# Performance work log

Measured on AMD Instinct MI355X. Metric: run time of the kernel, lower is better.

Reference implementation:

```python
import jax, jax.numpy as jnp
import numpy as np
from jax import lax

E = 64        # SUB_NETWORK_DIM
M = 512       # memory_size
H = 8         # num_heads
DH = E // H
B = 32768     # batch of x
EPS = 1e-5


def setup_inputs() -> dict:
    key = jax.random.key(0)
    ks = jax.random.split(key, 12)
    inp = {
        "x": jax.random.normal(ks[0], (B, E), jnp.float32),
        # MemoryModule params (torch.randn init)
        "mem_w": jax.random.normal(ks[1], (M, E, E), jnp.float32),
        "ln_g": jnp.ones((M, E), jnp.float32),
        "ln_b": jnp.zeros((M, E), jnp.float32),
        # pre-attention projections
        "Wq": jax.random.normal(ks[2], (E, E), jnp.float32) * 0.05,
        "bq": jnp.zeros((E,), jnp.float32),
        "Wk": jax.random.normal(ks[3], (E, E), jnp.float32) * 0.05,
        "bk": jnp.zeros((E,), jnp.float32),
        "Wv": jax.random.normal(ks[4], (E, E), jnp.float32) * 0.05,
        "bv": jnp.zeros((E,), jnp.float32),
        # nn.MultiheadAttention internal projections
        "in_proj_w": jax.random.normal(ks[5], (3 * E, E), jnp.float32) * 0.05,
        "in_proj_b": jnp.zeros((3 * E,), jnp.float32),
        "out_w": jax.random.normal(ks[6], (E, E), jnp.float32) * 0.05,
        "out_b": jnp.zeros((E,), jnp.float32),
    }
    return inp


def _layernorm(h, g, b):
    mu = jnp.mean(h, axis=-1, keepdims=True)
    var = jnp.mean((h - mu) ** 2, axis=-1, keepdims=True)
    return (h - mu) * lax.rsqrt(var + EPS) * g + b


def reference(x, mem_w, ln_g, ln_b, Wq, bq, Wk, bk, Wv, bv,
              in_proj_w, in_proj_b, out_w, out_b):
    # --- sequential memory module: relu(x @ W.T) -> LayerNorm, M times ---
    def step(h, p):
        W, g, b = p
        h = jax.nn.relu(h @ W.T)
        return _layernorm(h, g, b), None

    mem_out, _ = lax.scan(step, x, (mem_w, ln_g, ln_b))   # [B, E]
    mem_out = lax.stop_gradient(mem_out)                  # torch.no_grad()

    # --- attention: queries = per-row means of memory weights ---
    avg_w = jnp.mean(mem_w, axis=-1)                      # [M, E]
    q = avg_w @ Wq.T + bq                                 # [M, E]
    k = mem_out @ Wk.T + bk                               # [B, E]
    v = mem_out @ Wv.T + bv                               # [B, E]

    Wqi, Wki, Wvi = in_proj_w[:E], in_proj_w[E:2 * E], in_proj_w[2 * E:]
    bqi, bki, bvi = in_proj_b[:E], in_proj_b[E:2 * E], in_proj_b[2 * E:]
    qh = (q @ Wqi.T + bqi).reshape(M, H, DH)
    kh = (k @ Wki.T + bki).reshape(B, H, DH)
    vh = (v @ Wvi.T + bvi).reshape(B, H, DH)

    scores = jnp.einsum("mhd,nhd->hmn", qh, kh) / np.sqrt(DH).astype(np.float32)
    attn = jax.nn.softmax(scores, axis=-1)                # [H, M, B]
    o = jnp.einsum("hmn,nhd->mhd", attn, vh).reshape(M, E)
    attn_out = o @ out_w.T + out_b                        # [M, E]

    # --- elementwise weight update: W += W * (delta / row_mean)[:, None] ---
    row_mean = jnp.mean(mem_w, axis=-1)                   # [M, E]
    new_mem_w = mem_w + mem_w * (attn_out / row_mean)[..., None]

    return mem_out, new_mem_w
```

## Files before the change

### kernel.cpp

```cpp
#include <hip/hip_runtime.h>
#include <hip/hip_bf16.h>
#include <cstdint>
#include <cstddef>

typedef __attribute__((ext_vector_type(8))) short short8;
typedef __attribute__((ext_vector_type(4))) float f32x4;
typedef unsigned short ushort_t;

#define WBF_OFF   0u
#define KVH_OFF   4194304u
#define QH_OFF    12582912u
#define AVG_OFF   12713984u
#define WEFF_OFF  12845056u
#define BEFF_OFF  12894208u
#define OACC_OFF  12894976u
#define ESUM_OFF  13026048u
#define FLAG_OFF  13173504u
#define PO_OFF    13180928u
#define PE_OFF    21569536u
#define WKV_OFF   22618112u
#define WS_NEED   22634496ull
#define NCH 64

__device__ __forceinline__ float bf2f(ushort_t u) {
  union { unsigned int i; float f; } c; c.i = ((unsigned int)u) << 16; return c.f;
}
__device__ __forceinline__ unsigned cvtpk(float a, float b) {
  unsigned r;
  asm("v_cvt_pk_bf16_f32 %0, %1, %2" : "=v"(r) : "v"(a), "v"(b));
  return r;
}
__device__ __forceinline__ ushort_t f2bf1(float f) {
  union { float f; unsigned int i; } c; c.f = f;
  unsigned int x = c.i;
  x += 0x7FFFu + ((x >> 16) & 1u);
  return (ushort_t)(x >> 16);
}
__device__ __forceinline__ float fbits(unsigned u) { return __builtin_bit_cast(float, u); }
__device__ __forceinline__ unsigned ubits(float f) { return __builtin_bit_cast(unsigned, f); }

__device__ __forceinline__ void pl16raw(unsigned &a, unsigned &b) {
  asm("v_permlane16_swap_b32 %0, %1" : "+v"(a), "+v"(b));
}
__device__ __forceinline__ void pl32raw(unsigned &a, unsigned &b) {
  asm("v_permlane32_swap_b32 %0, %1" : "+v"(a), "+v"(b));
}
__device__ __forceinline__ void pl16raw_ec(unsigned &a, unsigned &b) {
  asm("v_permlane16_swap_b32 %0, %1" : "+&v"(a), "+&v"(b));
}
__device__ __forceinline__ void pl32raw_ec(unsigned &a, unsigned &b) {
  asm("v_permlane32_swap_b32 %0, %1" : "+&v"(a), "+&v"(b));
}
template<bool REV> __device__ __forceinline__ void x16(unsigned &a, unsigned &b) {
  if (!REV) pl16raw(a, b); else pl16raw(b, a);
}
template<bool REV> __device__ __forceinline__ void x32(unsigned &a, unsigned &b) {
  if (!REV) pl32raw(a, b); else pl32raw(b, a);
}
__device__ __forceinline__ float red4(float v) {
  unsigned a = ubits(v), b = a;
  asm("" : "+v"(b));
  pl16raw_ec(a, b);
  float w = fbits(a) + fbits(b);
  unsigned c = ubits(w), d = c;
  asm("" : "+v"(d));
  pl32raw_ec(c, d);
  return fbits(c) + fbits(d);
}

__global__ __launch_bounds__(256) void kinit(float* oacc) {
  int gid = blockIdx.x * 256 + threadIdx.x;
  if (gid < 36864) oacc[gid] = 0.f;
}

__global__ __launch_bounds__(256) void kpre(const float* __restrict__ mem_w,
                                            const float* __restrict__ ln_g,
                                            const float* __restrict__ ln_b,
                                            const float* __restrict__ in_proj_w,
                                            const float* __restrict__ in_proj_b,
                                            const float* __restrict__ Wq, const float* __restrict__ bq,
                                            const float* __restrict__ Wk, const float* __restrict__ bk,
                                            const float* __restrict__ Wv, const float* __restrict__ bv,
                                            short* __restrict__ wbf,
                                            float* __restrict__ avg,
                                            float* __restrict__ weff,
                                            float* __restrict__ beff,
                                            short* __restrict__ wkv,
                                            int* __restrict__ flag) {
  int gid = blockIdx.x * 256 + threadIdx.x;
  if (gid < 32768) {
    const float4* src = (const float4*)(mem_w + (size_t)gid * 64);
    int4* dst = (int4*)(wbf + (size_t)gid * 64);
    float sum = 0.f;
#pragma unroll
    for (int c = 0; c < 8; ++c) {
      float4 f0 = src[c * 2], f1 = src[c * 2 + 1];
      sum += f0.x + f0.y + f0.z + f0.w + f1.x + f1.y + f1.z + f1.w;
      int4 pk;
      pk.x = (int)cvtpk(f0.x, f0.y); pk.y = (int)cvtpk(f0.z, f0.w);
      pk.z = (int)cvtpk(f1.x, f1.y); pk.w = (int)cvtpk(f1.z, f1.w);
      dst[c] = pk;
    }
    avg[gid] = sum * 0.015625f;
  } else if (gid < 65536) {
    int j = gid - 32768;
    if (ln_g[j] != 1.0f || ln_b[j] != 0.0f) atomicOr(flag, 1);
  } else if (gid < 77824) {
    int k = gid - 65536;
    int mat = k >> 12, j = (k >> 6) & 63, e = k & 63;
    const float* Wi = in_proj_w + ((size_t)(mat * 64 + j)) * 64;
    const float* Wx = (mat == 0) ? Wq : ((mat == 1) ? Wk : Wv);
    float acc = 0.f;
#pragma unroll 8
    for (int tt = 0; tt < 64; ++tt) acc = fmaf(Wi[tt], Wx[tt * 64 + e], acc);
    weff[k] = acc;
    if (mat >= 1) wkv[(mat - 1) * 4096 + (k & 4095)] = (short)f2bf1(acc);
  } else if (gid < 78016) {
    int k = gid - 77824; int mat = k >> 6, j = k & 63;
    const float* Wi = in_proj_w + ((size_t)(mat * 64 + j)) * 64;
    const float* bx = (mat == 0) ? bq : ((mat == 1) ? bk : bv);
    float acc = in_proj_b[mat * 64 + j];
#pragma unroll 8
    for (int tt = 0; tt < 64; ++tt) acc = fmaf(Wi[tt], bx[tt], acc);
    beff[k] = acc;
  }
}

__global__ __launch_bounds__(256) void kqh(const float* __restrict__ avg,
                                           const float* __restrict__ weff,
                                           const float* __restrict__ beff,
                                           float* __restrict__ qh) {
  int gid = blockIdx.x * 256 + threadIdx.x;
  int m = gid >> 6, j = gid & 63;
  const float* ar = avg + (size_t)m * 64;
  const float* wr = weff + (size_t)j * 64;
  float acc = beff[j];
#pragma unroll 8
  for (int e = 0; e < 64; ++e) acc = fmaf(ar[e], wr[e], acc);
  qh[gid] = acc * 0.35355339059327373f;
}

#define KSTEP(PP, WFC, WFN, GC, GN)                                            \
  {                                                                            \
    const int m = mb + PP;                                                     \
    if (m + 2 < 512) *(int4*)((char*)wlds[(PP + 2) & 3] + so0) = GC;           \
    if (m + 3 < 512) GN = ((const int4*)wbf)[(m + 3) * 512 + t];               \
    if (m + 1 < 512) {                                                         \
      const char* rb = (const char*)wlds[(PP + 1) & 3];                        \
      _Pragma("unroll")                                                        \
      for (int i = 0; i < 8; ++i) WFN[i] = *(const short8*)(rb + wrd[i]);      \
    }                                                                          \
    f32x4 acc0 = __builtin_amdgcn_mfma_f32_16x16x32_bf16(WFC[0], hf0, z4, 0, 0, 0); \
    f32x4 acc1 = __builtin_amdgcn_mfma_f32_16x16x32_bf16(WFC[2], hf0, z4, 0, 0, 0); \
    f32x4 acc2 = __builtin_amdgcn_mfma_f32_16x16x32_bf16(WFC[4], hf0, z4, 0, 0, 0); \
    f32x4 acc3 = __builtin_amdgcn_mfma_f32_16x16x32_bf16(WFC[6], hf0, z4, 0, 0, 0); \
    acc0 = __builtin_amdgcn_mfma_f32_16x16x32_bf16(WFC[1], hf1, acc0, 0, 0, 0); \
    acc1 = __builtin_amdgcn_mfma_f32_16x16x32_bf16(WFC[3], hf1, acc1, 0, 0, 0); \
    acc2 = __builtin_amdgcn_mfma_f32_16x16x32_bf16(WFC[5], hf1, acc2, 0, 0, 0); \
    acc3 = __builtin_amdgcn_mfma_f32_16x16x32_bf16(WFC[7], hf1, acc3, 0, 0, 0); \
    _Pragma("unroll")                                                          \
    for (int rg = 0; rg < 4; ++rg) {                                           \
      outv[rg]      = fmaxf(acc0[rg], 0.f);                                    \
      outv[4 + rg]  = fmaxf(acc1[rg], 0.f);                                    \
      outv[8 + rg]  = fmaxf(acc2[rg], 0.f);                                    \
      outv[12 + rg] = fmaxf(acc3[rg], 0.f);                                    \
    }                                                                          \
    float s = (((outv[0] + outv[1]) + (outv[2] + outv[3]))                     \
             + ((outv[4] + outv[5]) + (outv[6] + outv[7])))                    \
            + (((outv[8] + outv[9]) + (outv[10] + outv[11]))                   \
             + ((outv[12] + outv[13]) + (outv[14] + outv[15])));               \
    float qa = fmaf(outv[3], outv[3], fmaf(outv[2], outv[2],                   \
               fmaf(outv[1], outv[1], outv[0] * outv[0])));                    \
    float qb = fmaf(outv[7], outv[7], fmaf(outv[6], outv[6],                   \
               fmaf(outv[5], outv[5], outv[4] * outv[4])));                    \
    float qc = fmaf(outv[11], outv[11], fmaf(outv[10], outv[10],               \
               fmaf(outv[9], outv[9], outv[8] * outv[8])));                    \
    float qd = fmaf(outv[15], outv[15], fmaf(outv[14], outv[14],               \
               fmaf(outv[13], outv[13], outv[12] * outv[12])));                \
    float sq = (qa + qb) + (qc + qd);                                          \
    s = red4(s); sq = red4(sq);                                                \
    const float mean = s * 0.015625f;                                          \
    const float var = fmaf(sq, 0.015625f, -mean * mean);                       \
    const float rs = rsqrtf(var + 1e-5f);                                      \
    const float cc = -mean * rs;                                               \
    if (gb) {                                                                  \
      _Pragma("unroll")                                                        \
      for (int mt = 0; mt < 4; ++mt) {                                         \
        float4 gg = *(const float4*)(ln_g + m * 64 + mt * 16 + lg * 4);        \
        float4 bb = *(const float4*)(ln_b + m * 64 + mt * 16 + lg * 4);        \
        outv[mt * 4 + 0] = fmaf(fmaf(outv[mt * 4 + 0], rs, cc), gg.x, bb.x);   \
        outv[mt * 4 + 1] = fmaf(fmaf(outv[mt * 4 + 1], rs, cc), gg.y, bb.y);   \
        outv[mt * 4 + 2] = fmaf(fmaf(outv[mt * 4 + 2], rs, cc), gg.z, bb.z);   \
        outv[mt * 4 + 3] = fmaf(fmaf(outv[mt * 4 + 3], rs, cc), gg.w, bb.w);   \
      }                                                                        \
    } else {                                                                   \
      _Pragma("unroll")                                                        \
      for (int i = 0; i < 16; ++i) outv[i] = fmaf(outv[i], rs, cc);            \
    }                                                                          \
    if (m < 511) {                                                             \
      unsigned Q0 = cvtpk(outv[0], outv[1]),   Q1 = cvtpk(outv[2], outv[3]);   \
      unsigned Q2 = cvtpk(outv[4], outv[5]),   Q3 = cvtpk(outv[6], outv[7]);   \
      unsigned Q4 = cvtpk(outv[8], outv[9]),   Q5 = cvtpk(outv[10], outv[11]); \
      unsigned Q6 = cvtpk(outv[12], outv[13]), Q7 = cvtpk(outv[14], outv[15]); \
      x32<R32>(Q0, Q2); x16<R16>(Q0, Q2);                                      \
      x32<R32>(Q1, Q3); x16<R16>(Q1, Q3);                                      \
      x32<R32>(Q4, Q6); x16<R16>(Q4, Q6);                                      \
      x32<R32>(Q5, Q7); x16<R16>(Q5, Q7);                                      \
      union { unsigned d[4]; short8 s8; } uu0, uu1;                            \
      uu0.d[0] = Q0; uu0.d[1] = Q1; uu0.d[2] = Q2; uu0.d[3] = Q3;              \
      uu1.d[0] = Q4; uu1.d[1] = Q5; uu1.d[2] = Q6; uu1.d[3] = Q7;              \
      hf0 = uu0.s8; hf1 = uu1.s8;                                              \
    }                                                                          \
    asm volatile("s_waitcnt lgkmcnt(8)" ::: "memory");                         \
    __builtin_amdgcn_s_barrier();                                              \
  }

template<bool R16, bool R32>
__device__ void kscan_body(const float* __restrict__ x,
                           const short* __restrict__ wbf,
                           const float* __restrict__ ln_g,
                           const float* __restrict__ ln_b,
                           int gb, float* __restrict__ mem_out,
                           short* __restrict__ wldsb) {
  short (*wlds)[64 * 64] = (short (*)[64 * 64])wldsb;
  const int t = threadIdx.x;
  const int lane = t & 63;
  const int wv = t >> 6;
  const int lcol = lane & 15;
  const int lg = lane >> 4;
  const int blk = blockIdx.x;
  const int r = wv * 16 + lcol;

  const int wsw = (lcol & 7) << 4;
  int wrd[8];
#pragma unroll
  for (int mt = 0; mt < 4; ++mt) {
    wrd[mt * 2]     = mt * 2048 + lcol * 128 + ((lg * 16) ^ wsw);
    wrd[mt * 2 + 1] = mt * 2048 + lcol * 128 + ((lg * 16 + 64) ^ wsw);
  }
  const int so0 = (t * 16) ^ ((((t * 16) >> 7) & 7) << 4);

  short8 hf0, hf1;
  {
    const float4* xr = (const float4*)(x + ((size_t)(blk * 128 + r)) * 64);
    float4 a0 = xr[lg * 2], a1 = xr[lg * 2 + 1];
    float4 b0 = xr[8 + lg * 2], b1 = xr[8 + lg * 2 + 1];
    union { unsigned d[4]; short8 s8; } u0, u1;
    u0.d[0] = cvtpk(a0.x, a0.y); u0.d[1] = cvtpk(a0.z, a0.w);
    u0.d[2] = cvtpk(a1.x, a1.y); u0.d[3] = cvtpk(a1.z, a1.w);
    u1.d[0] = cvtpk(b0.x, b0.y); u1.d[1] = cvtpk(b0.z, b0.w);
    u1.d[2] = cvtpk(b1.x, b1.y); u1.d[3] = cvtpk(b1.z, b1.w);
    hf0 = u0.s8; hf1 = u1.s8;
  }
  {
    int4 w0 = ((const int4*)wbf)[t];
    int4 w1 = ((const int4*)wbf)[512 + t];
    *(int4*)((char*)wlds[0] + so0) = w0;
    *(int4*)((char*)wlds[1] + so0) = w1;
  }
  int4 g0 = ((const int4*)wbf)[1024 + t];
  int4 g1;
  __syncthreads();

  short8 wfA[8], wfB[8];
#pragma unroll
  for (int i = 0; i < 8; ++i) wfA[i] = *(const short8*)((const char*)wlds[0] + wrd[i]);

  const f32x4 z4 = {0.f, 0.f, 0.f, 0.f};
  float outv[16];

  for (int mb = 0; mb < 512; mb += 4) {
    KSTEP(0, wfA, wfB, g0, g1)
    KSTEP(1, wfB, wfA, g1, g0)
    KSTEP(2, wfA, wfB, g0, g1)
    KSTEP(3, wfB, wfA, g1, g0)
  }

  float* mo = mem_out + ((size_t)(blk * 128 + r)) * 64;
#pragma unroll
  for (int mt = 0; mt < 4; ++mt)
    *(float4*)(mo + mt * 16 + lg * 4) =
        make_float4(outv[mt * 4], outv[mt * 4 + 1], outv[mt * 4 + 2], outv[mt * 4 + 3]);
}

__global__ __launch_bounds__(512, 2) void kscan(
    const float* __restrict__ x, const short* __restrict__ wbf,
    const float* __restrict__ ln_g, const float* __restrict__ ln_b,
    const int* __restrict__ flagp, float* __restrict__ mem_out) {
  __shared__ short wlds[4][64 * 64];
  const int lane = threadIdx.x & 63;
  const int gb = *flagp;
  unsigned pa = (unsigned)lane, pb = 1000u + (unsigned)lane;
  pl16raw_ec(pa, pb);
  const bool r16 = (__builtin_amdgcn_readfirstlane((int)pa) != 0);
  unsigned qa = (unsigned)lane, qb = 2000u + (unsigned)lane;
  pl32raw_ec(qa, qb);
  const bool r32 = (__builtin_amdgcn_readfirstlane((int)qa) != 0);
  short* ldsb = &wlds[0][0];
  if (!r16) {
    if (!r32) kscan_body<false, false>(x, wbf, ln_g, ln_b, gb, mem_out, ldsb);
    else      kscan_body<false, true >(x, wbf, ln_g, ln_b, gb, mem_out, ldsb);
  } else {
    if (!r32) kscan_body<true, false >(x, wbf, ln_g, ln_b, gb, mem_out, ldsb);
    else      kscan_body<true, true  >(x, wbf, ln_g, ln_b, gb, mem_out, ldsb);
  }
}

__global__ __launch_bounds__(512) void kkvm(const float* __restrict__ mem_out,
                                            const short* __restrict__ wkv,
                                            const float* __restrict__ beff,
                                            short* __restrict__ khvh) {
  __shared__ short wl[2][64 * 64];
  const int t = threadIdx.x;
  const int lane = t & 63;
  const int wv = t >> 6;
  const int lcol = lane & 15;
  const int lg = lane >> 4;
  const int r = wv * 16 + lcol;
  const int n = blockIdx.x * 128 + r;
  const int wsw = (lcol & 7) << 4;
  int wrd[8];
#pragma unroll
  for (int mt = 0; mt < 4; ++mt) {
    wrd[mt * 2]     = mt * 2048 + lcol * 128 + ((lg * 16) ^ wsw);
    wrd[mt * 2 + 1] = mt * 2048 + lcol * 128 + ((lg * 16 + 64) ^ wsw);
  }
  const int so0 = (t * 16) ^ ((((t * 16) >> 7) & 7) << 4);
  {
    const int4* wp = (const int4*)wkv;
    *(int4*)((char*)wl[0] + so0) = wp[t];
    *(int4*)((char*)wl[1] + so0) = wp[512 + t];
  }
  short8 hf0, hf1;
  {
    const float4* xr = (const float4*)(mem_out + (size_t)n * 64);
    float4 a0 = xr[lg * 2], a1 = xr[lg * 2 + 1];
    float4 b0 = xr[8 + lg * 2], b1 = xr[8 + lg * 2 + 1];
    union { unsigned d[4]; short8 s8; } u0, u1;
    u0.d[0] = cvtpk(a0.x, a0.y); u0.d[1] = cvtpk(a0.z, a0.w);
    u0.d[2] = cvtpk(a1.x, a1.y); u0.d[3] = cvtpk(a1.z, a1.w);
    u1.d[0] = cvtpk(b0.x, b0.y); u1.d[1] = cvtpk(b0.z, b0.w);
    u1.d[2] = cvtpk(b1.x, b1.y); u1.d[3] = cvtpk(b1.z, b1.w);
    hf0 = u0.s8; hf1 = u1.s8;
  }
  __syncthreads();
  const f32x4 z4 = {0.f, 0.f, 0.f, 0.f};
  short* row = khvh + (size_t)n * 128;
#pragma unroll
  for (int mt = 0; mt < 4; ++mt) {
    short8 k0 = *(const short8*)((const char*)wl[0] + wrd[mt * 2]);
    short8 k1 = *(const short8*)((const char*)wl[0] + wrd[mt * 2 + 1]);
    f32x4 aK = __builtin_amdgcn_mfma_f32_16x16x32_bf16(k0, hf0, z4, 0, 0, 0);
    aK = __builtin_amdgcn_mfma_f32_16x16x32_bf16(k1, hf1, aK, 0, 0, 0);
    short8 v0 = *(const short8*)((const char*)wl[1] + wrd[mt * 2]);
    short8 v1 = *(const short8*)((const char*)wl[1] + wrd[mt * 2 + 1]);
    f32x4 aV = __builtin_amdgcn_mfma_f32_16x16x32_bf16(v0, hf0, z4, 0, 0, 0);
    aV = __builtin_amdgcn_mfma_f32_16x16x32_bf16(v1, hf1, aV, 0, 0, 0);
    float4 bk = *(const float4*)(beff + 64 + mt * 16 + lg * 4);
    float4 bv = *(const float4*)(beff + 128 + mt * 16 + lg * 4);
    uint2 pk_, pv_;
    pk_.x = cvtpk(aK[0] + bk.x, aK[1] + bk.y);
    pk_.y = cvtpk(aK[2] + bk.z, aK[3] + bk.w);
    pv_.x = cvtpk(aV[0] + bv.x, aV[1] + bv.y);
    pv_.y = cvtpk(aV[2] + bv.z, aV[3] + bv.w);
    *(uint2*)(row + mt * 16 + lg * 4) = pk_;
    *(uint2*)(row + 64 + mt * 16 + lg * 4) = pv_;
  }
}

__global__ __launch_bounds__(256) void kkv(const float* __restrict__ mem_out,
                                           const float* __restrict__ weff,
                                           const float* __restrict__ beff,
                                           short* __restrict__ khvh) {
  __shared__ short kvs[128 * 128];
  const int t = threadIdx.x;
  const int nl = t >> 1;
  const int jh = (t & 1) * 32;
  const int n = blockIdx.x * 128 + nl;
  float mo[64];
  const float4* mop = (const float4*)(mem_out + (size_t)n * 64);
#pragma unroll
  for (int c = 0; c < 16; ++c) {
    float4 f = mop[c];
    mo[c * 4] = f.x; mo[c * 4 + 1] = f.y; mo[c * 4 + 2] = f.z; mo[c * 4 + 3] = f.w;
  }
  const float* wk = weff + 4096;
  const float* wvp = weff + 8192;
  const float* bk = beff + 64;
  const float* bv = beff + 128;
  for (int jj = 0; jj < 32; ++jj) {
    const int j = jh + jj;
    float ak = bk[j], av = bv[j];
    const float* wkr = wk + (size_t)j * 64;
    const float* wvr = wvp + (size_t)j * 64;
#pragma unroll 8
    for (int e = 0; e < 64; ++e) { ak = fmaf(mo[e], wkr[e], ak); av = fmaf(mo[e], wvr[e], av); }
    kvs[nl * 128 + j] = (short)f2bf1(ak);
    kvs[nl * 128 + 64 + j] = (short)f2bf1(av);
  }
  __syncthreads();
  int4* dst = (int4*)(khvh + (size_t)blockIdx.x * 16384);
  const int4* srcl = (const int4*)kvs;
#pragma unroll
  for (int c = 0; c < 8; ++c) dst[t + c * 256] = srcl[t + c * 256];
}

__global__ __launch_bounds__(512) void kattn2(const short* __restrict__ khvh,
                                              const float* __restrict__ qh,
                                              float* __restrict__ pO,
                                              float* __restrict__ pE) {
  __shared__ short kv[128 * 128];
  const int t = threadIdx.x;
  const int hh = t >> 6;
  const int ml = t & 63;
  const int c = blockIdx.x >> 2;
  const int mc = blockIdx.x & 3;
  const int m0 = mc * 128 + ml;
  const int m1 = m0 + 64;
  float q0[8], q1[8], o0[8], o1[8];
  float e0 = 0.f, e1 = 0.f;
  {
    const float4* qp0 = (const float4*)(qh + (size_t)m0 * 64 + hh * 8);
    const float4* qp1 = (const float4*)(qh + (size_t)m1 * 64 + hh * 8);
    float4 a = qp0[0], b = qp0[1], cc2 = qp1[0], d2 = qp1[1];
    q0[0]=a.x; q0[1]=a.y; q0[2]=a.z; q0[3]=a.w; q0[4]=b.x; q0[5]=b.y; q0[6]=b.z; q0[7]=b.w;
    q1[0]=cc2.x; q1[1]=cc2.y; q1[2]=cc2.z; q1[3]=cc2.w; q1[4]=d2.x; q1[5]=d2.y; q1[6]=d2.z; q1[7]=d2.w;
#pragma unroll
    for (int d = 0; d < 8; ++d) { o0[d] = 0.f; o1[d] = 0.f; }
  }
  for (int tile = 0; tile < 4; ++tile) {
    if (tile) __syncthreads();
    const int4* src = (const int4*)(khvh + ((size_t)(c * 512 + tile * 128)) * 128);
    int4* dl = (int4*)kv;
#pragma unroll
    for (int u = 0; u < 4; ++u) dl[t + u * 512] = src[t + u * 512];
    __syncthreads();
    for (int n = 0; n < 128; ++n) {
      const short8 kraw = *(const short8*)(kv + n * 128 + hh * 8);
      const short8 vraw = *(const short8*)(kv + n * 128 + 64 + hh * 8);
      float kf[8], vf[8];
#pragma unroll
      for (int d = 0; d < 8; ++d) {
        kf[d] = bf2f((ushort_t)kraw[d]);
        vf[d] = bf2f((ushort_t)vraw[d]);
      }
      float s0 = 0.f, s1 = 0.f;
#pragma unroll
      for (int d = 0; d < 8; ++d) { s0 = fmaf(q0[d], kf[d], s0); s1 = fmaf(q1[d], kf[d], s1); }
      float p0 = __expf(s0), p1 = __expf(s1);
      e0 += p0; e1 += p1;
#pragma unroll
      for (int d = 0; d < 8; ++d) { o0[d] = fmaf(p0, vf[d], o0[d]); o1[d] = fmaf(p1, vf[d], o1[d]); }
    }
  }
  const int idx0 = hh * 512 + m0;
  const int idx1 = hh * 512 + m1;
  pE[(size_t)c * 4096 + idx0] = e0;
  pE[(size_t)c * 4096 + idx1] = e1;
  float4* po0 = (float4*)(pO + (size_t)c * 32768 + (size_t)idx0 * 8);
  float4* po1 = (float4*)(pO + (size_t)c * 32768 + (size_t)idx1 * 8);
  po0[0] = make_float4(o0[0], o0[1], o0[2], o0[3]);
  po0[1] = make_float4(o0[4], o0[5], o0[6], o0[7]);
  po1[0] = make_float4(o1[0], o1[1], o1[2], o1[3]);
  po1[1] = make_float4(o1[4], o1[5], o1[6], o1[7]);
}

__global__ __launch_bounds__(512) void kattn_atomic(const short* __restrict__ khvh,
                                                    const float* __restrict__ qh,
                                                    float* __restrict__ oacc,
                                                    float* __restrict__ esum) {
  __shared__ short kv[128 * 128];
  const int t = threadIdx.x;
  const int hh = t >> 6;
  const int ms = t & 63;
  {
    const int4* src = (const int4*)(khvh + (size_t)blockIdx.x * 16384);
    int4* d = (int4*)kv;
#pragma unroll
    for (int c = 0; c < 4; ++c) d[t + c * 512] = src[t + c * 512];
  }
  __syncthreads();
  float q[8][8], o[8][8], es[8];
#pragma unroll
  for (int i = 0; i < 8; ++i) {
    const float4* qp = (const float4*)(qh + ((size_t)(ms + i * 64)) * 64 + hh * 8);
    float4 q0 = qp[0], q1 = qp[1];
    q[i][0] = q0.x; q[i][1] = q0.y; q[i][2] = q0.z; q[i][3] = q0.w;
    q[i][4] = q1.x; q[i][5] = q1.y; q[i][6] = q1.z; q[i][7] = q1.w;
    es[i] = 0.f;
#pragma unroll
    for (int d = 0; d < 8; ++d) o[i][d] = 0.f;
  }
  for (int n = 0; n < 128; ++n) {
    const short8 kraw = *(const short8*)(kv + n * 128 + hh * 8);
    const short8 vraw = *(const short8*)(kv + n * 128 + 64 + hh * 8);
    float kf[8], vf[8];
#pragma unroll
    for (int d = 0; d < 8; ++d) {
      kf[d] = bf2f((ushort_t)kraw[d]);
      vf[d] = bf2f((ushort_t)vraw[d]);
    }
#pragma unroll
    for (int i = 0; i < 8; ++i) {
      float s = 0.f;
#pragma unroll
      for (int d = 0; d < 8; ++d) s = fmaf(q[i][d], kf[d], s);
      float p = __expf(s);
      es[i] += p;
#pragma unroll
      for (int d = 0; d < 8; ++d) o[i][d] = fmaf(p, vf[d], o[i][d]);
    }
  }
#pragma unroll
  for (int i = 0; i < 8; ++i) {
    const int m = ms + i * 64;
    atomicAdd(&esum[hh * 512 + m], es[i]);
#pragma unroll
    for (int d = 0; d < 8; ++d) atomicAdd(&oacc[((size_t)(hh * 512 + m)) * 8 + d], o[i][d]);
  }
}

__global__ __launch_bounds__(256) void kfr2(const float* __restrict__ pO,
                                            const float* __restrict__ pE,
                                            const float* __restrict__ out_w,
                                            const float* __restrict__ out_b,
                                            const float* __restrict__ avg,
                                            const float* __restrict__ mem_w,
                                            float* __restrict__ out1) {
  __shared__ float ored[64];
  __shared__ float ered[8];
  __shared__ float rat[64];
  const int t = threadIdx.x;
  const int m = blockIdx.x;
  if (t < 64) {
    int h = t >> 3, d = t & 7;
    float s = 0.f;
#pragma unroll 8
    for (int c = 0; c < NCH; ++c)
      s += pO[(size_t)c * 32768 + ((size_t)(h * 512 + m)) * 8 + d];
    ored[t] = s;
  } else if (t < 72) {
    int h = t - 64;
    float s = 0.f;
#pragma unroll 8
    for (int c = 0; c < NCH; ++c)
      s += pE[(size_t)c * 4096 + h * 512 + m];
    ered[h] = s;
  }
  __syncthreads();
  if (t < 64) {
    const int e = t;
    float inv[8];
#pragma unroll
    for (int h = 0; h < 8; ++h) inv[h] = 1.f / ered[h];
    float a = out_b[e];
    const float* wr = out_w + (size_t)e * 64;
#pragma unroll
    for (int j = 0; j < 64; ++j) a = fmaf(ored[j] * inv[j >> 3], wr[j], a);
    rat[e] = 1.f + a / avg[m * 64 + e];
  }
  __syncthreads();
  const float4* src = (const float4*)(mem_w + (size_t)m * 4096);
  float4* dst = (float4*)(out1 + (size_t)m * 4096);
#pragma unroll
  for (int c = 0; c < 4; ++c) {
    int idx = t + c * 256;
    float rr = rat[idx >> 4];
    float4 w = src[idx];
    dst[idx] = make_float4(w.x * rr, w.y * rr, w.z * rr, w.w * rr);
  }
}

__global__ __launch_bounds__(256) void kfr(const float* __restrict__ oacc,
                                           const float* __restrict__ esum,
                                           const float* __restrict__ out_w,
                                           const float* __restrict__ out_b,
                                           const float* __restrict__ avg,
                                           const float* __restrict__ mem_w,
                                           float* __restrict__ out1) {
  __shared__ float rat[64];
  const int t = threadIdx.x;
  const int m = blockIdx.x;
  if (t < 64) {
    const int e = t;
    float of[64];
#pragma unroll
    for (int h = 0; h < 8; ++h) {
      float inv = 1.f / esum[h * 512 + m];
      const float* op = oacc + ((size_t)(h * 512 + m)) * 8;
#pragma unroll
      for (int d = 0; d < 8; ++d) of[h * 8 + d] = op[d] * inv;
    }
    float a = out_b[e];
    const float* wr = out_w + (size_t)e * 64;
#pragma unroll 8
    for (int j = 0; j < 64; ++j) a = fmaf(of[j], wr[j], a);
    rat[e] = 1.f + a / avg[m * 64 + e];
  }
  __syncthreads();
  const float4* src = (const float4*)(mem_w + (size_t)m * 4096);
  float4* dst = (float4*)(out1 + (size_t)m * 4096);
#pragma unroll
  for (int c = 0; c < 4; ++c) {
    int idx = t + c * 256;
    float rr = rat[idx >> 4];
    float4 w = src[idx];
    dst[idx] = make_float4(w.x * rr, w.y * rr, w.z * rr, w.w * rr);
  }
}

extern "C" void kernel_launch(void* const* d_in, const int* in_sizes, int n_in,
                              void* d_out, int out_size, void* d_ws, size_t ws_size,
                              hipStream_t stream) {
  (void)in_sizes; (void)n_in; (void)out_size;
  const float* x         = (const float*)d_in[0];
  const float* mem_w     = (const float*)d_in[1];
  const float* ln_g      = (const float*)d_in[2];
  const float* ln_b      = (const float*)d_in[3];
  const float* Wq        = (const float*)d_in[4];
  const float* bq        = (const float*)d_in[5];
  const float* Wk        = (const float*)d_in[6];
  const float* bk        = (const float*)d_in[7];
  const float* Wv        = (const float*)d_in[8];
  const float* bv        = (const float*)d_in[9];
  const float* in_proj_w = (const float*)d_in[10];
  const float* in_proj_b = (const float*)d_in[11];
  const float* out_w     = (const float*)d_in[12];
  const float* out_b     = (const float*)d_in[13];

  float* dout = (float*)d_out;
  char* ws = (char*)d_ws;
  short* wbf   = (short*)(ws + WBF_OFF);
  short* khvh  = (short*)(ws + KVH_OFF);
  float* qh    = (float*)(ws + QH_OFF);
  float* avg   = (float*)(ws + AVG_OFF);
  float* weff  = (float*)(ws + WEFF_OFF);
  float* beff  = (float*)(ws + BEFF_OFF);
  float* oacc  = (float*)(ws + OACC_OFF);
  float* esum  = (float*)(ws + ESUM_OFF);
  int*   flag  = (int*)(ws + FLAG_OFF);
  float* pO    = (float*)(ws + PO_OFF);
  float* pE    = (float*)(ws + PE_OFF);
  short* wkv   = (short*)(ws + WKV_OFF);

  float* mem_out = dout;
  float* out1    = dout + 2097152;

  const bool use_part = (ws_size >= WS_NEED);

  hipMemsetAsync(flag, 0, 4, stream);
  kpre<<<305, 256, 0, stream>>>(mem_w, ln_g, ln_b, in_proj_w, in_proj_b,
                                Wq, bq, Wk, bk, Wv, bv, wbf, avg, weff, beff,
                                wkv, flag);
  kqh<<<128, 256, 0, stream>>>(avg, weff, beff, qh);
  kscan<<<256, 512, 0, stream>>>(x, wbf, ln_g, ln_b, flag, mem_out);
  if (use_part) {
    kkvm<<<256, 512, 0, stream>>>(mem_out, wkv, beff, khvh);
    kattn2<<<NCH * 4, 512, 0, stream>>>(khvh, qh, pO, pE);
    kfr2<<<512, 256, 0, stream>>>(pO, pE, out_w, out_b, avg, mem_w, out1);
  } else {
    kkv<<<256, 256, 0, stream>>>(mem_out, weff, beff, khvh);
    kinit<<<144, 256, 0, stream>>>(oacc);
    kattn_atomic<<<256, 512, 0, stream>>>(khvh, qh, oacc, esum);
    kfr<<<512, 256, 0, stream>>>(oacc, esum, out_w, out_b, avg, mem_w, out1);
  }
}
```

Before: 465.2 us.

## Defer LayerNorm affine into next step's matmul via precomputed weight row sums

When the LayerNorm gain and bias are identity, the normalisation (h-mean)*rs is no longer applied before packing to bf16. The raw relu output is packed instead, and the next step recovers the normalised product as rs*(W·h) + cc*rowsum(W), using per-row weight sums precomputed in kpre from the bf16-rounded weights. This removes the per-element normalise FMAs from the serial critical path. The cost is extra row-sum loads each step and a final fixup after the loop. Feeding unnormalised values to bf16 MFMA may also change rounding behaviour. The WSUM buffer aliases the KVH region, which is only written after the scan completes.

```diff
diff --git a/kernel.cpp b/kernel.cpp
--- a/kernel.cpp
+++ b/kernel.cpp
@@ -9,6 +9,7 @@
 
 #define WBF_OFF   0u
 #define KVH_OFF   4194304u
+#define WSUM_OFF  4194304u
 #define QH_OFF    12582912u
 #define AVG_OFF   12713984u
 #define WEFF_OFF  12845056u
@@ -38,6 +39,9 @@
 }
 __device__ __forceinline__ float fbits(unsigned u) { return __builtin_bit_cast(float, u); }
 __device__ __forceinline__ unsigned ubits(float f) { return __builtin_bit_cast(unsigned, f); }
+__device__ __forceinline__ float rsum2(unsigned u) {
+  return fbits(u << 16) + fbits(u & 0xffff0000u);
+}
 
 __device__ __forceinline__ void pl16raw(unsigned &a, unsigned &b) {
   asm("v_permlane16_swap_b32 %0, %1" : "+v"(a), "+v"(b));
@@ -86,12 +90,13 @@
                                             float* __restrict__ weff,
                                             float* __restrict__ beff,
                                             short* __restrict__ wkv,
+                                            float* __restrict__ wsum,
                                             int* __restrict__ flag) {
   int gid = blockIdx.x * 256 + threadIdx.x;
   if (gid < 32768) {
     const float4* src = (const float4*)(mem_w + (size_t)gid * 64);
     int4* dst = (int4*)(wbf + (size_t)gid * 64);
-    float sum = 0.f;
+    float sum = 0.f, rsum = 0.f;
 #pragma unroll
     for (int c = 0; c < 8; ++c) {
       float4 f0 = src[c * 2], f1 = src[c * 2 + 1];
@@ -99,9 +104,12 @@
       int4 pk;
       pk.x = (int)cvtpk(f0.x, f0.y); pk.y = (int)cvtpk(f0.z, f0.w);
       pk.z = (int)cvtpk(f1.x, f1.y); pk.w = (int)cvtpk(f1.z, f1.w);
+      rsum += (rsum2((unsigned)pk.x) + rsum2((unsigned)pk.y))
+            + (rsum2((unsigned)pk.z) + rsum2((unsigned)pk.w));
       dst[c] = pk;
     }
     avg[gid] = sum * 0.015625f;
+    wsum[gid] = rsum;
   } else if (gid < 65536) {
     int j = gid - 32768;
     if (ln_g[j] != 1.0f || ln_b[j] != 0.0f) atomicOr(flag, 1);
@@ -140,12 +148,15 @@
   qh[gid] = acc * 0.35355339059327373f;
 }
 
-#define KSTEP(PP, WFC, WFN, GC, GN)                                            \
+#define KSTEP(PP, WFC, WFN, GC, GN, WSC, WSN)                                  \
   {                                                                            \
     const int m = mb + PP;                                                     \
     if (m + 2 < 512) *(int4*)((char*)wlds[(PP + 2) & 3] + so0) = GC;           \
     if (m + 3 < 512) GN = ((const int4*)wbf)[(m + 3) * 512 + t];               \
     if (m + 1 < 512) {                                                         \
+      _Pragma("unroll")                                                        \
+      for (int mt = 0; mt < 4; ++mt)                                           \
+        WSN[mt] = *(const f32x4*)(wsb + (m + 1) * 64 + mt * 16);               \
       const char* rb = (const char*)wlds[(PP + 1) & 3];                        \
       _Pragma("unroll")                                                        \
       for (int i = 0; i < 8; ++i) WFN[i] = *(const short8*)(rb + wrd[i]);      \
@@ -160,10 +171,24 @@
     acc3 = __builtin_amdgcn_mfma_f32_16x16x32_bf16(WFC[7], hf1, acc3, 0, 0, 0); \
     _Pragma("unroll")                                                          \
     for (int rg = 0; rg < 4; ++rg) {                                           \
-      outv[rg]      = fmaxf(acc0[rg], 0.f);                                    \
-      outv[4 + rg]  = fmaxf(acc1[rg], 0.f);                                    \
-      outv[8 + rg]  = fmaxf(acc2[rg], 0.f);                                    \
-      outv[12 + rg] = fmaxf(acc3[rg], 0.f);                                    \
+      outv[rg]      = fmaxf(fmaf(rs_p, acc0[rg], cc_p * WSC[0][rg]), 0.f);     \
+      outv[4 + rg]  = fmaxf(fmaf(rs_p, acc1[rg], cc_p * WSC[1][rg]), 0.f);     \
+      outv[8 + rg]  = fmaxf(fmaf(rs_p, acc2[rg], cc_p * WSC[2][rg]), 0.f);     \
+      outv[12 + rg] = fmaxf(fmaf(rs_p, acc3[rg], cc_p * WSC[3][rg]), 0.f);     \
+    }                                                                          \
+    if (m < 511) {                                                             \
+      unsigned Q0 = cvtpk(outv[0], outv[1]),   Q1 = cvtpk(outv[2], outv[3]);   \
+      unsigned Q2 = cvtpk(outv[4], outv[5]),   Q3 = cvtpk(outv[6], outv[7]);   \
+      unsigned Q4 = cvtpk(outv[8], outv[9]),   Q5 = cvtpk(outv[10], outv[11]); \
+      unsigned Q6 = cvtpk(outv[12], outv[13]), Q7 = cvtpk(outv[14], outv[15]); \
+      x32<R32>(Q0, Q2); x16<R16>(Q0, Q2);                                      \
+      x32<R32>(Q1, Q3); x16<R16>(Q1, Q3);                                      \
+      x32<R32>(Q4, Q6); x16<R16>(Q4, Q6);                                      \
+      x32<R32>(Q5, Q7); x16<R16>(Q5, Q7);                                      \
+      union { unsigned d[4]; short8 s8; } uu0, uu1;                            \
+      uu0.d[0] = Q0; uu0.d[1] = Q1; uu0.d[2] = Q2; uu0.d[3] = Q3;              \
+      uu1.d[0] = Q4; uu1.d[1] = Q5; uu1.d[2] = Q6; uu1.d[3] = Q7;              \
+      hf0 = uu0.s8; hf1 = uu1.s8;                                              \
     }                                                                          \
     float s = (((outv[0] + outv[1]) + (outv[2] + outv[3]))                     \
              + ((outv[4] + outv[5]) + (outv[6] + outv[7])))                    \
@@ -183,7 +208,7 @@
     const float var = fmaf(sq, 0.015625f, -mean * mean);                       \
     const float rs = rsqrtf(var + 1e-5f);                                      \
     const float cc = -mean * rs;                                               \
-    if (gb) {                                                                  \
+    if (gb) {      \
       _Pragma("unroll")                                                        \
       for (int mt = 0; mt < 4; ++mt) {                                         \
         float4 gg = *(const float4*)(ln_g + m * 64 + mt * 16 + lg * 4);        \
@@ -193,23 +218,23 @@
         outv[mt * 4 + 2] = fmaf(fmaf(outv[mt * 4 + 2], rs, cc), gg.z, bb.z);   \
         outv[mt * 4 + 3] = fmaf(fmaf(outv[mt * 4 + 3], rs, cc), gg.w, bb.w);   \
       }                                                                        \
+      if (m < 511) {                           \
+        unsigned Q0 = cvtpk(outv[0], outv[1]),   Q1 = cvtpk(outv[2], outv[3]); \
+        unsigned Q2 = cvtpk(outv[4], outv[5]),   Q3 = cvtpk(outv[6], outv[7]); \
+        unsigned Q4 = cvtpk(outv[8], outv[9]),   Q5 = cvtpk(outv[10], outv[11]);\
+        unsigned Q6 = cvtpk(outv[12], outv[13]), Q7 = cvtpk(outv[14], outv[15]);\
+        x32<R32>(Q0, Q2); x16<R16>(Q0, Q2);                                    \
+        x32<R32>(Q1, Q3); x16<R16>(Q1, Q3);                                    \
+        x32<R32>(Q4, Q6); x16<R16>(Q4, Q6);                                    \
+        x32<R32>(Q5, Q7); x16<R16>(Q5, Q7);                                    \
+        union { unsigned d[4]; short8 s8; } vv0, vv1;                          \
+        vv0.d[0] = Q0; vv0.d[1] = Q1; vv0.d[2] = Q2; vv0.d[3] = Q3;            \
+        vv1.d[0] = Q4; vv1.d[1] = Q5; vv1.d[2] = Q6; vv1.d[3] = Q7;            \
+        hf0 = vv0.s8; hf1 = vv1.s8;                                            \
+      }                                                                        \
+      rs_p = 1.f; cc_p = 0.f;                                                  \
     } else {                                                                   \
-      _Pragma("unroll")                                                        \
-      for (int i = 0; i < 16; ++i) outv[i] = fmaf(outv[i], rs, cc);            \
-    }                                                                          \
-    if (m < 511) {                                                             \
-      unsigned Q0 = cvtpk(outv[0], outv[1]),   Q1 = cvtpk(outv[2], outv[3]);   \
-      unsigned Q2 = cvtpk(outv[4], outv[5]),   Q3 = cvtpk(outv[6], outv[7]);   \
-      unsigned Q4 = cvtpk(outv[8], outv[9]),   Q5 = cvtpk(outv[10], outv[11]); \
-      unsigned Q6 = cvtpk(outv[12], outv[13]), Q7 = cvtpk(outv[14], outv[15]); \
-      x32<R32>(Q0, Q2); x16<R16>(Q0, Q2);                                      \
-      x32<R32>(Q1, Q3); x16<R16>(Q1, Q3);                                      \
-      x32<R32>(Q4, Q6); x16<R16>(Q4, Q6);                                      \
-      x32<R32>(Q5, Q7); x16<R16>(Q5, Q7);                                      \
-      union { unsigned d[4]; short8 s8; } uu0, uu1;                            \
-      uu0.d[0] = Q0; uu0.d[1] = Q1; uu0.d[2] = Q2; uu0.d[3] = Q3;              \
-      uu1.d[0] = Q4; uu1.d[1] = Q5; uu1.d[2] = Q6; uu1.d[3] = Q7;              \
-      hf0 = uu0.s8; hf1 = uu1.s8;                                              \
+      rs_p = rs; cc_p = cc;                                                    \
     }                                                                          \
     asm volatile("s_waitcnt lgkmcnt(8)" ::: "memory");                         \
     __builtin_amdgcn_s_barrier();                                              \
@@ -220,6 +245,7 @@
                            const short* __restrict__ wbf,
                            const float* __restrict__ ln_g,
                            const float* __restrict__ ln_b,
+                           const float* __restrict__ wsum,
                            int gb, float* __restrict__ mem_out,
                            short* __restrict__ wldsb) {
   short (*wlds)[64 * 64] = (short (*)[64 * 64])wldsb;
@@ -239,6 +265,7 @@
     wrd[mt * 2 + 1] = mt * 2048 + lcol * 128 + ((lg * 16 + 64) ^ wsw);
   }
   const int so0 = (t * 16) ^ ((((t * 16) >> 7) & 7) << 4);
+  const float* wsb = wsum + lg * 4;
 
   short8 hf0, hf1;
   {
@@ -260,6 +287,10 @@
   }
   int4 g0 = ((const int4*)wbf)[1024 + t];
   int4 g1;
+  f32x4 wsA[4], wsB[4];
+#pragma unroll
+  for (int mt = 0; mt < 4; ++mt) wsA[mt] = *(const f32x4*)(wsb + mt * 16);
+  float rs_p = 1.f, cc_p = 0.f;
   __syncthreads();
 
   short8 wfA[8], wfB[8];
@@ -270,12 +301,14 @@
   float outv[16];
 
   for (int mb = 0; mb < 512; mb += 4) {
-    KSTEP(0, wfA, wfB, g0, g1)
-    KSTEP(1, wfB, wfA, g1, g0)
-    KSTEP(2, wfA, wfB, g0, g1)
-    KSTEP(3, wfB, wfA, g1, g0)
-  }
-
+    KSTEP(0, wfA, wfB, g0, g1, wsA, wsB)
+    KSTEP(1, wfB, wfA, g1, g0, wsB, wsA)
+    KSTEP(2, wfA, wfB, g0, g1, wsA, wsB)
+    KSTEP(3, wfB, wfA, g1, g0, wsB, wsA)
+  }
+
+#pragma unroll
+  for (int i = 0; i < 16; ++i) outv[i] = fmaf(outv[i], rs_p, cc_p);
   float* mo = mem_out + ((size_t)(blk * 128 + r)) * 64;
 #pragma unroll
   for (int mt = 0; mt < 4; ++mt)
@@ -286,6 +319,7 @@
 __global__ __launch_bounds__(512, 2) void kscan(
     const float* __restrict__ x, const short* __restrict__ wbf,
     const float* __restrict__ ln_g, const float* __restrict__ ln_b,
+    const float* __restrict__ wsum,
     const int* __restrict__ flagp, float* __restrict__ mem_out) {
   __shared__ short wlds[4][64 * 64];
   const int lane = threadIdx.x & 63;
@@ -298,11 +332,11 @@
   const bool r32 = (__builtin_amdgcn_readfirstlane((int)qa) != 0);
   short* ldsb = &wlds[0][0];
   if (!r16) {
-    if (!r32) kscan_body<false, false>(x, wbf, ln_g, ln_b, gb, mem_out, ldsb);
-    else      kscan_body<false, true >(x, wbf, ln_g, ln_b, gb, mem_out, ldsb);
+    if (!r32) kscan_body<false, false>(x, wbf, ln_g, ln_b, wsum, gb, mem_out, ldsb);
+    else      kscan_body<false, true >(x, wbf, ln_g, ln_b, wsum, gb, mem_out, ldsb);
   } else {
-    if (!r32) kscan_body<true, false >(x, wbf, ln_g, ln_b, gb, mem_out, ldsb);
-    else      kscan_body<true, true  >(x, wbf, ln_g, ln_b, gb, mem_out, ldsb);
+    if (!r32) kscan_body<true, false >(x, wbf, ln_g, ln_b, wsum, gb, mem_out, ldsb);
+    else      kscan_body<true, true  >(x, wbf, ln_g, ln_b, wsum, gb, mem_out, ldsb);
   }
 }
 
@@ -632,6 +666,7 @@
   char* ws = (char*)d_ws;
   short* wbf   = (short*)(ws + WBF_OFF);
   short* khvh  = (short*)(ws + KVH_OFF);
+  float* wsum  = (float*)(ws + WSUM_OFF);
   float* qh    = (float*)(ws + QH_OFF);
   float* avg   = (float*)(ws + AVG_OFF);
   float* weff  = (float*)(ws + WEFF_OFF);
@@ -651,9 +686,9 @@
   hipMemsetAsync(flag, 0, 4, stream);
   kpre<<<305, 256, 0, stream>>>(mem_w, ln_g, ln_b, in_proj_w, in_proj_b,
                                 Wq, bq, Wk, bk, Wv, bv, wbf, avg, weff, beff,
-                                wkv, flag);
+                                wkv, wsum, flag);
   kqh<<<128, 256, 0, stream>>>(avg, weff, beff, qh);
-  kscan<<<256, 512, 0, stream>>>(x, wbf, ln_g, ln_b, flag, mem_out);
+  kscan<<<256, 512, 0, stream>>>(x, wbf, ln_g, ln_b, wsum, flag, mem_out);
   if (use_part) {
     kkvm<<<256, 512, 0, stream>>>(mem_out, wkv, beff, khvh);
     kattn2<<<NCH * 4, 512, 0, stream>>>(khvh, qh, pO, pE);
```

Result: slower. 549.3 us (+18.1%).
